# Kernel tuning notes

Measured on AMD Instinct MI355X. Metric: run time of the kernel, lower is better.

Reference implementation:

```python
import jax, jax.numpy as jnp
import numpy as np

B, S, D = 2, 8192, 1024
H, HD, FD = 16, 64, 256

def setup_inputs() -> dict:
    key = jax.random.key(0)
    ks = jax.random.split(key, 6)
    sc = 1.0 / np.sqrt(D)
    return {
        "hidden_states": jax.random.normal(ks[0], (B, S, D), jnp.float32),
        "Wq": jax.random.normal(ks[1], (D, D), jnp.float32) * sc,
        "Wk": jax.random.normal(ks[2], (D, D), jnp.float32) * sc,
        "Wv": jax.random.normal(ks[3], (D, D), jnp.float32) * sc,
        "Wo": jax.random.normal(ks[4], (D, D), jnp.float32) * sc,
        "Wf": jax.random.normal(ks[5], (FD, HD), jnp.float32) * (1.0 / np.sqrt(HD)),
    }

def reference(hidden_states, Wq, Wk, Wv, Wo, Wf):
    b, s, _ = hidden_states.shape
    # projections (torch Linear: x @ W.T), split heads -> (b, s, h, hd)
    q = (hidden_states @ Wq.T).reshape(b, s, H, HD)
    k = (hidden_states @ Wk.T).reshape(b, s, H, HD)
    v = (hidden_states @ Wv.T).reshape(b, s, H, HD)
    # elu+1 feature map -> (b, s, h, f)
    qf = jax.nn.elu(q @ Wf.T) + 1.0
    kf = jax.nn.elu(k @ Wf.T) + 1.0
    # global kv summary: (b, h, f, d)
    kv = jnp.einsum('bshf,bshd->bhfd', kf, v)
    out = jnp.einsum('bshf,bhfd->bshd', qf, kv)
    k_sum = kf.sum(axis=1)                       # (b, h, f)
    norm = jnp.einsum('bshf,bhf->bsh', qf, k_sum)[..., None] + 1e-6
    out = (out / norm).reshape(b, s, D)
    return out @ Wo.T
```

## Files before the change

kernel.cpp:

```cpp
#include <hip/hip_runtime.h>
#include <stdint.h>

typedef __bf16 bf16_t;
typedef __attribute__((ext_vector_type(8))) __bf16 bfv8;
typedef __attribute__((ext_vector_type(4))) __bf16 bfv4;
typedef __attribute__((ext_vector_type(4))) float f32x4;

constexpr int BATCH = 2, SEQ = 8192, DIM = 1024, NH = 16, HDIM = 64, FDIM = 256;
constexpr int MROWS = BATCH * SEQ;
constexpr int NCHUNK = 16;
constexpr int KV_NIT = (SEQ / NCHUNK) / 32;
constexpr int KVP_CH = 32 * 256 * 68;

__device__ __forceinline__ f32x4 mfma_bf16(bfv8 a, bfv8 b, f32x4 c) {
  return __builtin_amdgcn_mfma_f32_16x16x32_bf16(a, b, c, 0, 0, 0);
}

__device__ __forceinline__ void gload_lds16(const bf16_t* g, bf16_t* lds) {
  auto const* gp = reinterpret_cast<const __attribute__((address_space(1))) uint32_t*>(
      reinterpret_cast<uintptr_t>(g));
  auto* lp = reinterpret_cast<__attribute__((address_space(3))) uint32_t*>(
      reinterpret_cast<uintptr_t>(lds));
  __builtin_amdgcn_global_load_lds(gp, lp, 16, 0, 0);
}

__device__ __forceinline__ void stage128x64(const bf16_t* g_base, int k0,
                                            bf16_t* lds, int wid, int lane) {
#pragma unroll
  for (int j = 0; j < 4; ++j) {
    int r0 = (wid * 4 + j) * 8;
    int g_row = r0 + (lane >> 3);
    int g_slot = (lane & 7) ^ (g_row & 7);
    const bf16_t* src = g_base + (size_t)g_row * DIM + k0 + g_slot * 8;
    gload_lds16(src, lds + r0 * 64);
  }
}

__global__ __launch_bounds__(256) void cvt_all(const float* __restrict__ X,
                                               const float* __restrict__ Wq,
                                               const float* __restrict__ Wk,
                                               const float* __restrict__ Wv,
                                               const float* __restrict__ Wo,
                                               const float* __restrict__ Wf,
                                               bf16_t* __restrict__ Xb,
                                               bf16_t* __restrict__ W3,
                                               bf16_t* __restrict__ Wob,
                                               bf16_t* __restrict__ Wfb) {
  int i = blockIdx.x * 256 + threadIdx.x;
  const float* src;
  bf16_t* dst;
  int off;
  if (i < 4194304) {
    src = X; dst = Xb; off = i;
  } else {
    int j = i - 4194304;
    if (j < 786432) {
      int seg = j >> 18;
      off = j & 262143;
      src = (seg == 0) ? Wq : ((seg == 1) ? Wk : Wv);
      dst = W3 + (size_t)seg * 1048576;
    } else if (j < 1048576) {
      off = j - 786432; src = Wo; dst = Wob;
    } else {
      off = j - 1048576; src = Wf; dst = Wfb;
    }
  }
  float4 v = reinterpret_cast<const float4*>(src)[off];
  bfv4 o = {(__bf16)v.x, (__bf16)v.y, (__bf16)v.z, (__bf16)v.w};
  reinterpret_cast<bfv4*>(dst)[off] = o;
}

__global__ __launch_bounds__(256) void gemm_qkv(const bf16_t* __restrict__ A,
                                                const bf16_t* __restrict__ Wall,
                                                bf16_t* __restrict__ Q,
                                                bf16_t* __restrict__ K,
                                                bf16_t* __restrict__ V) {
  __shared__ bf16_t As[2][128 * 64];
  __shared__ bf16_t Bs[2][128 * 64];
  int bid = blockIdx.x;
  int xcd = bid & 7, s = bid >> 3;
  int pair = xcd * 48 + (s >> 3);
  int z = pair >> 7, bx = pair & 127, by = s & 7;
  const bf16_t* Wm = Wall + (size_t)z * (DIM * DIM);
  bf16_t* C = (z == 0) ? Q : ((z == 1) ? K : V);
  int lane = threadIdx.x & 63, wid = threadIdx.x >> 6;
  int lr = lane & 15, lg = lane >> 4;
  int wr = wid >> 1, wc = wid & 1;
  int brow = bx * 128, bcol = by * 128;
  const bf16_t* Ab = A + (size_t)brow * DIM;
  const bf16_t* Bb = Wm + (size_t)bcol * DIM;
  f32x4 acc[4][4] = {};

  stage128x64(Ab, 0, As[0], wid, lane);
  stage128x64(Bb, 0, Bs[0], wid, lane);
  asm volatile("s_waitcnt vmcnt(0)" ::: "memory");
  __builtin_amdgcn_s_barrier();

  auto TILE = [&](const bf16_t* Acur, const bf16_t* Bcur, bf16_t* Anext, bf16_t* Bnext,
                  int knext) __attribute__((always_inline)) {
    if (knext < DIM) {
      stage128x64(Ab, knext, Anext, wid, lane);
      stage128x64(Bb, knext, Bnext, wid, lane);
    }
#pragma unroll
    for (int kk = 0; kk < 2; ++kk) {
      bfv8 af[4], bg[4];
#pragma unroll
      for (int t = 0; t < 4; ++t) {
        int ar = wr * 64 + t * 16 + lr;
        af[t] = *reinterpret_cast<const bfv8*>(&Acur[ar * 64 + (((kk * 4 + lg) ^ (ar & 7)) * 8)]);
        int br = wc * 64 + t * 16 + lr;
        bg[t] = *reinterpret_cast<const bfv8*>(&Bcur[br * 64 + (((kk * 4 + lg) ^ (br & 7)) * 8)]);
      }
#pragma unroll
      for (int i = 0; i < 4; ++i)
#pragma unroll
        for (int j = 0; j < 4; ++j) acc[i][j] = mfma_bf16(af[i], bg[j], acc[i][j]);
    }
    asm volatile("s_waitcnt vmcnt(0)" ::: "memory");
    __builtin_amdgcn_s_barrier();
  };

  for (int ks = 0; ks < DIM / 64; ks += 2) {
    TILE(As[0], Bs[0], As[1], Bs[1], (ks + 1) * 64);
    TILE(As[1], Bs[1], As[0], Bs[0], (ks + 2) * 64);
  }

#pragma unroll
  for (int i = 0; i < 4; ++i) {
    int r = brow + wr * 64 + i * 16 + lg * 4;
#pragma unroll
    for (int j = 0; j < 4; ++j) {
      int c = bcol + wc * 64 + j * 16 + lr;
#pragma unroll
      for (int q = 0; q < 4; ++q) C[(size_t)(r + q) * DIM + c] = (__bf16)acc[i][j][q];
    }
  }
}

__global__ __launch_bounds__(256) void gemm_final(const bf16_t* __restrict__ A,
                                                  const bf16_t* __restrict__ W,
                                                  float* __restrict__ C) {
  __shared__ bf16_t As[2][128 * 64];
  __shared__ bf16_t Bs[2][128 * 64];
  int bid = blockIdx.x;
  int xcd = bid & 7, s = bid >> 3;
  int bx = xcd * 16 + (s >> 3);
  int by = s & 7;
  int lane = threadIdx.x & 63, wid = threadIdx.x >> 6;
  int lr = lane & 15, lg = lane >> 4;
  int wr = wid >> 1, wc = wid & 1;
  int brow = bx * 128, bcol = by * 128;
  const bf16_t* Ab = A + (size_t)brow * DIM;
  const bf16_t* Bb = W + (size_t)bcol * DIM;
  f32x4 acc[4][4] = {};

  stage128x64(Ab, 0, As[0], wid, lane);
  stage128x64(Bb, 0, Bs[0], wid, lane);
  asm volatile("s_waitcnt vmcnt(0)" ::: "memory");
  __builtin_amdgcn_s_barrier();

  auto TILE = [&](const bf16_t* Acur, const bf16_t* Bcur, bf16_t* Anext, bf16_t* Bnext,
                  int knext) __attribute__((always_inline)) {
    if (knext < DIM) {
      stage128x64(Ab, knext, Anext, wid, lane);
      stage128x64(Bb, knext, Bnext, wid, lane);
    }
#pragma unroll
    for (int kk = 0; kk < 2; ++kk) {
      bfv8 af[4], bg[4];
#pragma unroll
      for (int t = 0; t < 4; ++t) {
        int ar = wr * 64 + t * 16 + lr;
        af[t] = *reinterpret_cast<const bfv8*>(&Acur[ar * 64 + (((kk * 4 + lg) ^ (ar & 7)) * 8)]);
        int br = wc * 64 + t * 16 + lr;
        bg[t] = *reinterpret_cast<const bfv8*>(&Bcur[br * 64 + (((kk * 4 + lg) ^ (br & 7)) * 8)]);
      }
#pragma unroll
      for (int i = 0; i < 4; ++i)
#pragma unroll
        for (int j = 0; j < 4; ++j) acc[i][j] = mfma_bf16(af[i], bg[j], acc[i][j]);
    }
    asm volatile("s_waitcnt vmcnt(0)" ::: "memory");
    __builtin_amdgcn_s_barrier();
  };

  for (int ks = 0; ks < DIM / 64; ks += 2) {
    TILE(As[0], Bs[0], As[1], Bs[1], (ks + 1) * 64);
    TILE(As[1], Bs[1], As[0], Bs[0], (ks + 2) * 64);
  }

#pragma unroll
  for (int i = 0; i < 4; ++i) {
    int r = brow + wr * 64 + i * 16 + lg * 4;
#pragma unroll
    for (int j = 0; j < 4; ++j) {
      int c = bcol + wc * 64 + j * 16 + lr;
#pragma unroll
      for (int q = 0; q < 4; ++q) C[(size_t)(r + q) * DIM + c] = acc[i][j][q];
    }
  }
}

__global__ __launch_bounds__(256, 2) void kv_fused(const bf16_t* __restrict__ Kb,
                                                   const bf16_t* __restrict__ Vb,
                                                   const bf16_t* __restrict__ Wf,
                                                   float* __restrict__ kv_part) {
  __shared__ bf16_t vt[4][64 * 36];
  int chunk = blockIdx.x, bh = blockIdx.y;
  int b = bh >> 4, h = bh & 15;
  int lane = threadIdx.x & 63, wid = threadIdx.x >> 6;
  int lr = lane & 15, lg = lane >> 4;
  int f0 = wid * 64;
  bfv8 wf[4][2];
#pragma unroll
  for (int ft = 0; ft < 4; ++ft)
#pragma unroll
    for (int kk = 0; kk < 2; ++kk)
      wf[ft][kk] = *reinterpret_cast<const bfv8*>(Wf + (size_t)(f0 + ft * 16 + lr) * HDIM + kk * 32 + lg * 8);
  const bf16_t* Kbase = Kb + (size_t)b * SEQ * DIM + h * HDIM;
  const bf16_t* Vbase = Vb + (size_t)b * SEQ * DIM + h * HDIM;
  int s0 = chunk * (SEQ / NCHUNK);
  bfv8 ones;
#pragma unroll
  for (int j = 0; j < 8; ++j) ones[j] = (lr == 0) ? (__bf16)1.0f : (__bf16)0.0f;

  bfv8 krgA[2][2], krgB[2][2];
#pragma unroll
  for (int st = 0; st < 2; ++st)
#pragma unroll
    for (int kk = 0; kk < 2; ++kk)
      krgA[st][kk] = *reinterpret_cast<const bfv8*>(Kbase + (size_t)(s0 + st * 16 + lr) * DIM + kk * 32 + lg * 8);

  f32x4 acc[4][5] = {};

  auto STEP = [&](int it, bfv8(&krgC)[2][2], bfv8(&krgN)[2][2]) __attribute__((always_inline)) {
    int sb = s0 + it * 32;
    bfv8 vv[4];
#pragma unroll
    for (int rep = 0; rep < 4; ++rep) {
      int idx = rep * 64 + lane;
      vv[rep] = *reinterpret_cast<const bfv8*>(Vbase + (size_t)(sb + (idx >> 3)) * DIM + (idx & 7) * 8);
    }
    if (it + 1 < KV_NIT) {
#pragma unroll
      for (int st = 0; st < 2; ++st)
#pragma unroll
        for (int kk = 0; kk < 2; ++kk)
          krgN[st][kk] = *reinterpret_cast<const bfv8*>(Kbase + (size_t)(sb + 32 + st * 16 + lr) * DIM + kk * 32 + lg * 8);
    }
    f32x4 ckf[2][4] = {};
#pragma unroll
    for (int st = 0; st < 2; ++st)
#pragma unroll
      for (int ft = 0; ft < 4; ++ft)
#pragma unroll
        for (int kk = 0; kk < 2; ++kk) ckf[st][ft] = mfma_bf16(krgC[st][kk], wf[ft][kk], ckf[st][ft]);
#pragma unroll
    for (int rep = 0; rep < 4; ++rep) {
      int idx = rep * 64 + lane;
#pragma unroll
      for (int j = 0; j < 8; ++j) vt[wid][((idx & 7) * 8 + j) * 36 + (idx >> 3)] = vv[rep][j];
    }
    bfv8 af[4];
#pragma unroll
    for (int ft = 0; ft < 4; ++ft)
#pragma unroll
      for (int st = 0; st < 2; ++st)
#pragma unroll
        for (int q = 0; q < 4; ++q) {
          float x = ckf[st][ft][q];
          x = (x > 0.0f) ? (x + 1.0f) : __expf(x);
          af[ft][st * 4 + q] = (__bf16)x;
        }
    bfv8 bg[4];
#pragma unroll
    for (int nt = 0; nt < 4; ++nt) {
      bfv4 lo = *reinterpret_cast<const bfv4*>(&vt[wid][(nt * 16 + lr) * 36 + lg * 4]);
      bfv4 hi = *reinterpret_cast<const bfv4*>(&vt[wid][(nt * 16 + lr) * 36 + 16 + lg * 4]);
#pragma unroll
      for (int e = 0; e < 4; ++e) { bg[nt][e] = lo[e]; bg[nt][4 + e] = hi[e]; }
    }
#pragma unroll
    for (int ft = 0; ft < 4; ++ft) {
#pragma unroll
      for (int nt = 0; nt < 4; ++nt) acc[ft][nt] = mfma_bf16(af[ft], bg[nt], acc[ft][nt]);
      acc[ft][4] = mfma_bf16(af[ft], ones, acc[ft][4]);
    }
  };

  for (int it2 = 0; it2 < KV_NIT; it2 += 2) {
    STEP(it2, krgA, krgB);
    STEP(it2 + 1, krgB, krgA);
  }

  float* outb = kv_part + ((size_t)chunk * 32 + bh) * (FDIM * 68);
#pragma unroll
  for (int ft = 0; ft < 4; ++ft)
#pragma unroll
    for (int q = 0; q < 4; ++q) {
      int f = f0 + ft * 16 + lg * 4 + q;
#pragma unroll
      for (int nt = 0; nt < 4; ++nt)
        outb[(size_t)f * 68 + nt * 16 + lr] = acc[ft][nt][q];
      if (lr < 4) outb[(size_t)f * 68 + 64 + lr] = acc[ft][4][q];
    }
}

__global__ __launch_bounds__(256) void kv_reduce(const float* __restrict__ part,
                                                 bf16_t* __restrict__ kvT) {
  int i = blockIdx.x * 256 + threadIdx.x;
  if (i < KVP_CH) {
    int n = i % 68;
    int t = i / 68;
    int f = t & 255, bh = t >> 8;
    float s = 0.0f;
#pragma unroll
    for (int c = 0; c < NCHUNK; ++c) s += part[(size_t)c * KVP_CH + i];
    int fs = ((((f >> 3) ^ (n & 7)) << 3) | (f & 7));
    kvT[((size_t)bh * 80 + n) * FDIM + fs] = (__bf16)s;
  } else {
    int j = i - KVP_CH;
    int f = j & 255;
    int t = j >> 8;
    int n = 68 + t % 12, bh = t / 12;
    kvT[((size_t)bh * 80 + n) * FDIM + f] = (__bf16)0.0f;
  }
}

__global__ __launch_bounds__(256) void attn_fused(const bf16_t* __restrict__ Qb,
                                                  const bf16_t* __restrict__ Wf,
                                                  const bf16_t* __restrict__ kvT,
                                                  bf16_t* __restrict__ outp) {
  __shared__ bf16_t qf_lds[64 * 264];
  __shared__ bf16_t kv_lds[80 * 256];
  int rb = blockIdx.x, h = blockIdx.y;
  int row0 = rb * 64;
  int bh = (row0 >> 13) * NH + h;
  int lane = threadIdx.x & 63, wid = threadIdx.x >> 6;
  int lr = lane & 15, lg = lane >> 4;
  int f0 = wid * 64;
  const bf16_t* kvTb = kvT + (size_t)bh * 80 * FDIM;
#pragma unroll
  for (int i = 0; i < 10; ++i) {
    int sbase = wid * 640 + i * 64;
    gload_lds16(kvTb + (size_t)(sbase + lane) * 8, kv_lds + sbase * 8);
  }
  bfv8 qa[4][2], wfb[4][2];
#pragma unroll
  for (int t = 0; t < 4; ++t)
#pragma unroll
    for (int kk = 0; kk < 2; ++kk) {
      qa[t][kk] = *reinterpret_cast<const bfv8*>(Qb + (size_t)(row0 + t * 16 + lr) * DIM + h * HDIM + kk * 32 + lg * 8);
      wfb[t][kk] = *reinterpret_cast<const bfv8*>(Wf + (size_t)(f0 + t * 16 + lr) * HDIM + kk * 32 + lg * 8);
    }
  f32x4 cq[4][4] = {};
#pragma unroll
  for (int rt = 0; rt < 4; ++rt)
#pragma unroll
    for (int ft = 0; ft < 4; ++ft)
#pragma unroll
      for (int kk = 0; kk < 2; ++kk) cq[rt][ft] = mfma_bf16(qa[rt][kk], wfb[ft][kk], cq[rt][ft]);
#pragma unroll
  for (int rt = 0; rt < 4; ++rt)
#pragma unroll
    for (int ft = 0; ft < 4; ++ft)
#pragma unroll
      for (int q = 0; q < 4; ++q) {
        float x = cq[rt][ft][q];
        x = (x > 0.0f) ? (x + 1.0f) : __expf(x);
        qf_lds[(size_t)(rt * 16 + lg * 4 + q) * 264 + f0 + ft * 16 + lr] = (__bf16)x;
      }
  __syncthreads();
  f32x4 acc[5] = {};
#pragma unroll
  for (int ks = 0; ks < 8; ++ks) {
    bfv8 a = *reinterpret_cast<const bfv8*>(&qf_lds[(size_t)(wid * 16 + lr) * 264 + ks * 32 + lg * 8]);
#pragma unroll
    for (int nt = 0; nt < 5; ++nt) {
      bfv8 bg = *reinterpret_cast<const bfv8*>(
          &kv_lds[(size_t)(nt * 16 + lr) * 256 + (((ks * 4 + lg) ^ (lr & 7)) * 8)]);
      acc[nt] = mfma_bf16(a, bg, acc[nt]);
    }
  }
  __syncthreads();
#pragma unroll
  for (int q = 0; q < 4; ++q) {
    float nrm = __shfl(acc[4][q], (lane & 48)) + 1e-6f;
    int row = wid * 16 + lg * 4 + q;
#pragma unroll
    for (int nt = 0; nt < 4; ++nt)
      qf_lds[(size_t)row * 264 + nt * 16 + lr] = (__bf16)(acc[nt][q] / nrm);
  }
  __syncthreads();
#pragma unroll
  for (int rep = 0; rep < 2; ++rep) {
    int id = rep * 256 + threadIdx.x;
    int row = id >> 3, c8 = id & 7;
    bfv8 v = *reinterpret_cast<const bfv8*>(&qf_lds[(size_t)row * 264 + c8 * 8]);
    *reinterpret_cast<bfv8*>(&outp[(size_t)(row0 + row) * DIM + h * HDIM + c8 * 8]) = v;
  }
}

extern "C" void kernel_launch(void* const* d_in, const int* in_sizes, int n_in,
                              void* d_out, int out_size, void* d_ws, size_t ws_size,
                              hipStream_t stream) {
  const float* X  = (const float*)d_in[0];
  const float* Wq = (const float*)d_in[1];
  const float* Wk = (const float*)d_in[2];
  const float* Wv = (const float*)d_in[3];
  const float* Wo = (const float*)d_in[4];
  const float* Wf = (const float*)d_in[5];
  float* out = (float*)d_out;
  char* ws = (char*)d_ws;
  const size_t MB = 1ull << 20;
  if (ws_size < 75 * MB) return;

  bf16_t* Xb  = (bf16_t*)(ws + 0 * MB);
  bf16_t* W3  = (bf16_t*)(ws + 32 * MB);
  bf16_t* Qb  = (bf16_t*)(ws + 38 * MB);
  bf16_t* Wob = (bf16_t*)(ws + 70 * MB);
  bf16_t* Wfb = (bf16_t*)(ws + 72 * MB);
  bf16_t* kvT = (bf16_t*)(ws + 73 * MB);
  float* kv_part = (float*)(ws + 0 * MB);
  bf16_t* outp = (bf16_t*)(ws + 0 * MB);
  bf16_t* Kb = (bf16_t*)d_out;
  bf16_t* Vb = Kb + (size_t)MROWS * DIM;

  cvt_all<<<20496, 256, 0, stream>>>(X, Wq, Wk, Wv, Wo, Wf, Xb, W3, Wob, Wfb);

  gemm_qkv<<<3072, 256, 0, stream>>>(Xb, W3, Qb, Kb, Vb);
  kv_fused<<<dim3(NCHUNK, 32), 256, 0, stream>>>(Kb, Vb, Wfb, kv_part);
  kv_reduce<<<2560, 256, 0, stream>>>(kv_part, kvT);
  attn_fused<<<dim3(256, NH), 256, 0, stream>>>(Qb, Wfb, kvT, outp);
  gemm_final<<<1024, 256, 0, stream>>>(outp, Wob, out);
}
```

Measured before the change: 277.8 us.

## Store KV partials in fp16, double chunks, and process two row tiles per attention block

Three separate changes. The KV partial sums are now written and read as fp16 instead of fp32, which halves that intermediate traffic, and the number of sequence chunks doubles to 32, so kv_fused gets more blocks with shorter loops. attn_fused now handles 128 rows per block in two 64-row passes, so each kv_lds tile and set of Wf fragments loaded per block is reused twice and half as many blocks are launched. fp16 partials may lose precision or overflow for large values, and the larger attention tile adds an extra barrier per pass and halves the block count.

```diff
diff --git a/kernel.cpp b/kernel.cpp
--- a/kernel.cpp
+++ b/kernel.cpp
@@ -1,4 +1,5 @@
 #include <hip/hip_runtime.h>
+#include <hip/hip_fp16.h>
 #include <stdint.h>
 
 typedef __bf16 bf16_t;
@@ -8,7 +9,7 @@
 
 constexpr int BATCH = 2, SEQ = 8192, DIM = 1024, NH = 16, HDIM = 64, FDIM = 256;
 constexpr int MROWS = BATCH * SEQ;
-constexpr int NCHUNK = 16;
+constexpr int NCHUNK = 32;
 constexpr int KV_NIT = (SEQ / NCHUNK) / 32;
 constexpr int KVP_CH = 32 * 256 * 68;
 
@@ -205,7 +206,7 @@
 __global__ __launch_bounds__(256, 2) void kv_fused(const bf16_t* __restrict__ Kb,
                                                    const bf16_t* __restrict__ Vb,
                                                    const bf16_t* __restrict__ Wf,
-                                                   float* __restrict__ kv_part) {
+                                                   __half* __restrict__ kv_part) {
   __shared__ bf16_t vt[4][64 * 36];
   int chunk = blockIdx.x, bh = blockIdx.y;
   int b = bh >> 4, h = bh & 15;
@@ -294,7 +295,7 @@
     STEP(it2 + 1, krgB, krgA);
   }
 
-  float* outb = kv_part + ((size_t)chunk * 32 + bh) * (FDIM * 68);
+  __half* outb = kv_part + ((size_t)chunk * 32 + bh) * (FDIM * 68);
 #pragma unroll
   for (int ft = 0; ft < 4; ++ft)
 #pragma unroll
@@ -302,12 +303,12 @@
       int f = f0 + ft * 16 + lg * 4 + q;
 #pragma unroll
       for (int nt = 0; nt < 4; ++nt)
-        outb[(size_t)f * 68 + nt * 16 + lr] = acc[ft][nt][q];
-      if (lr < 4) outb[(size_t)f * 68 + 64 + lr] = acc[ft][4][q];
-    }
-}
-
-__global__ __launch_bounds__(256) void kv_reduce(const float* __restrict__ part,
+        outb[(size_t)f * 68 + nt * 16 + lr] = __float2half(acc[ft][nt][q]);
+      if (lr < 4) outb[(size_t)f * 68 + 64 + lr] = __float2half(acc[ft][4][q]);
+    }
+}
+
+__global__ __launch_bounds__(256) void kv_reduce(const __half* __restrict__ part,
                                                  bf16_t* __restrict__ kvT) {
   int i = blockIdx.x * 256 + threadIdx.x;
   if (i < KVP_CH) {
@@ -316,7 +317,7 @@
     int f = t & 255, bh = t >> 8;
     float s = 0.0f;
 #pragma unroll
-    for (int c = 0; c < NCHUNK; ++c) s += part[(size_t)c * KVP_CH + i];
+    for (int c = 0; c < NCHUNK; ++c) s += __half2float(part[(size_t)c * KVP_CH + i]);
     int fs = ((((f >> 3) ^ (n & 7)) << 3) | (f & 7));
     kvT[((size_t)bh * 80 + n) * FDIM + fs] = (__bf16)s;
   } else {
@@ -335,8 +336,8 @@
   __shared__ bf16_t qf_lds[64 * 264];
   __shared__ bf16_t kv_lds[80 * 256];
   int rb = blockIdx.x, h = blockIdx.y;
-  int row0 = rb * 64;
-  int bh = (row0 >> 13) * NH + h;
+  int row00 = rb * 128;
+  int bh = (row00 >> 13) * NH + h;
   int lane = threadIdx.x & 63, wid = threadIdx.x >> 6;
   int lr = lane & 15, lg = lane >> 4;
   int f0 = wid * 64;
@@ -346,59 +347,69 @@
     int sbase = wid * 640 + i * 64;
     gload_lds16(kvTb + (size_t)(sbase + lane) * 8, kv_lds + sbase * 8);
   }
-  bfv8 qa[4][2], wfb[4][2];
+  bfv8 wfb[4][2];
 #pragma unroll
   for (int t = 0; t < 4; ++t)
 #pragma unroll
-    for (int kk = 0; kk < 2; ++kk) {
-      qa[t][kk] = *reinterpret_cast<const bfv8*>(Qb + (size_t)(row0 + t * 16 + lr) * DIM + h * HDIM + kk * 32 + lg * 8);
+    for (int kk = 0; kk < 2; ++kk)
       wfb[t][kk] = *reinterpret_cast<const bfv8*>(Wf + (size_t)(f0 + t * 16 + lr) * HDIM + kk * 32 + lg * 8);
-    }
-  f32x4 cq[4][4] = {};
-#pragma unroll
-  for (int rt = 0; rt < 4; ++rt)
-#pragma unroll
-    for (int ft = 0; ft < 4; ++ft)
-#pragma unroll
-      for (int kk = 0; kk < 2; ++kk) cq[rt][ft] = mfma_bf16(qa[rt][kk], wfb[ft][kk], cq[rt][ft]);
-#pragma unroll
-  for (int rt = 0; rt < 4; ++rt)
-#pragma unroll
-    for (int ft = 0; ft < 4; ++ft)
-#pragma unroll
-      for (int q = 0; q < 4; ++q) {
-        float x = cq[rt][ft][q];
-        x = (x > 0.0f) ? (x + 1.0f) : __expf(x);
-        qf_lds[(size_t)(rt * 16 + lg * 4 + q) * 264 + f0 + ft * 16 + lr] = (__bf16)x;
+
+#pragma unroll
+  for (int sub = 0; sub < 2; ++sub) {
+    int row0 = row00 + sub * 64;
+    bfv8 qa[4][2];
+#pragma unroll
+    for (int t = 0; t < 4; ++t)
+#pragma unroll
+      for (int kk = 0; kk < 2; ++kk)
+        qa[t][kk] = *reinterpret_cast<const bfv8*>(Qb + (size_t)(row0 + t * 16 + lr) * DIM + h * HDIM + kk * 32 + lg * 8);
+    f32x4 cq[4][4] = {};
+#pragma unroll
+    for (int rt = 0; rt < 4; ++rt)
+#pragma unroll
+      for (int ft = 0; ft < 4; ++ft)
+#pragma unroll
+        for (int kk = 0; kk < 2; ++kk) cq[rt][ft] = mfma_bf16(qa[rt][kk], wfb[ft][kk], cq[rt][ft]);
+#pragma unroll
+    for (int rt = 0; rt < 4; ++rt)
+#pragma unroll
+      for (int ft = 0; ft < 4; ++ft)
+#pragma unroll
+        for (int q = 0; q < 4; ++q) {
+          float x = cq[rt][ft][q];
+          x = (x > 0.0f) ? (x + 1.0f) : __expf(x);
+          qf_lds[(size_t)(rt * 16 + lg * 4 + q) * 264 + f0 + ft * 16 + lr] = (__bf16)x;
+        }
+    __syncthreads();
+    f32x4 acc[5] = {};
+#pragma unroll
+    for (int ks = 0; ks < 8; ++ks) {
+      bfv8 a = *reinterpret_cast<const bfv8*>(&qf_lds[(size_t)(wid * 16 + lr) * 264 + ks * 32 + lg * 8]);
+#pragma unroll
+      for (int nt = 0; nt < 5; ++nt) {
+        bfv8 bg = *reinterpret_cast<const bfv8*>(
+            &kv_lds[(size_t)(nt * 16 + lr) * 256 + (((ks * 4 + lg) ^ (lr & 7)) * 8)]);
+        acc[nt] = mfma_bf16(a, bg, acc[nt]);
       }
-  __syncthreads();
-  f32x4 acc[5] = {};
-#pragma unroll
-  for (int ks = 0; ks < 8; ++ks) {
-    bfv8 a = *reinterpret_cast<const bfv8*>(&qf_lds[(size_t)(wid * 16 + lr) * 264 + ks * 32 + lg * 8]);
-#pragma unroll
-    for (int nt = 0; nt < 5; ++nt) {
-      bfv8 bg = *reinterpret_cast<const bfv8*>(
-          &kv_lds[(size_t)(nt * 16 + lr) * 256 + (((ks * 4 + lg) ^ (lr & 7)) * 8)]);
-      acc[nt] = mfma_bf16(a, bg, acc[nt]);
-    }
-  }
-  __syncthreads();
-#pragma unroll
-  for (int q = 0; q < 4; ++q) {
-    float nrm = __shfl(acc[4][q], (lane & 48)) + 1e-6f;
-    int row = wid * 16 + lg * 4 + q;
-#pragma unroll
-    for (int nt = 0; nt < 4; ++nt)
-      qf_lds[(size_t)row * 264 + nt * 16 + lr] = (__bf16)(acc[nt][q] / nrm);
-  }
-  __syncthreads();
-#pragma unroll
-  for (int rep = 0; rep < 2; ++rep) {
-    int id = rep * 256 + threadIdx.x;
-    int row = id >> 3, c8 = id & 7;
-    bfv8 v = *reinterpret_cast<const bfv8*>(&qf_lds[(size_t)row * 264 + c8 * 8]);
-    *reinterpret_cast<bfv8*>(&outp[(size_t)(row0 + row) * DIM + h * HDIM + c8 * 8]) = v;
+    }
+    __syncthreads();
+#pragma unroll
+    for (int q = 0; q < 4; ++q) {
+      float nrm = __shfl(acc[4][q], (lane & 48)) + 1e-6f;
+      int row = wid * 16 + lg * 4 + q;
+#pragma unroll
+      for (int nt = 0; nt < 4; ++nt)
+        qf_lds[(size_t)row * 264 + nt * 16 + lr] = (__bf16)(acc[nt][q] / nrm);
+    }
+    __syncthreads();
+#pragma unroll
+    for (int rep = 0; rep < 2; ++rep) {
+      int id = rep * 256 + threadIdx.x;
+      int row = id >> 3, c8 = id & 7;
+      bfv8 v = *reinterpret_cast<const bfv8*>(&qf_lds[(size_t)row * 264 + c8 * 8]);
+      *reinterpret_cast<bfv8*>(&outp[(size_t)(row0 + row) * DIM + h * HDIM + c8 * 8]) = v;
+    }
+    __syncthreads();
   }
 }
 
@@ -422,7 +433,7 @@
   bf16_t* Wob = (bf16_t*)(ws + 70 * MB);
   bf16_t* Wfb = (bf16_t*)(ws + 72 * MB);
   bf16_t* kvT = (bf16_t*)(ws + 73 * MB);
-  float* kv_part = (float*)(ws + 0 * MB);
+  __half* kv_part = (__half*)(ws + 0 * MB);
   bf16_t* outp = (bf16_t*)(ws + 0 * MB);
   bf16_t* Kb = (bf16_t*)d_out;
   bf16_t* Vb = Kb + (size_t)MROWS * DIM;
@@ -432,6 +443,6 @@
   gemm_qkv<<<3072, 256, 0, stream>>>(Xb, W3, Qb, Kb, Vb);
   kv_fused<<<dim3(NCHUNK, 32), 256, 0, stream>>>(Kb, Vb, Wfb, kv_part);
   kv_reduce<<<2560, 256, 0, stream>>>(kv_part, kvT);
-  attn_fused<<<dim3(256, NH), 256, 0, stream>>>(Qb, Wfb, kvT, outp);
+  attn_fused<<<dim3(128, NH), 256, 0, stream>>>(Qb, Wfb, kvT, outp);
   gemm_final<<<1024, 256, 0, stream>>>(outp, Wob, out);
 }
```

Result: faster. 272.3 us, median of 3 (-2.0%).
